# Performance work log

Measured on AMD Instinct MI355X. Metric: run time of the kernel, lower is better.

## Reference

```python
import jax, jax.numpy as jnp
import numpy as np


def setup_inputs() -> dict:
    key = jax.random.key(0)
    k1, k2, k3 = jax.random.split(key, 3)
    B, C, H, W = 64, 1024, 32, 32
    x = jax.random.normal(k1, (B, C, H, W), dtype=jnp.float32)
    # Conv2d(C, 1, kernel_size=1): weight [1, C, 1, 1] -> flatten to [C], bias [1] -> scalar
    bound = 1.0 / np.sqrt(C)
    attn_w = jax.random.uniform(k2, (C,), dtype=jnp.float32, minval=-bound, maxval=bound)
    attn_b = jax.random.uniform(k3, (), dtype=jnp.float32, minval=-bound, maxval=bound)
    return {"x": x, "attn_w": attn_w, "attn_b": attn_b}


def reference(x, attn_w, attn_b):
    B, C, H, W = x.shape
    # 1x1 conv producing one channel: score[b,h,w] = sum_c x[b,c,h,w]*w[c] + b
    scores = jnp.einsum('bchw,c->bhw', x, attn_w) + attn_b          # [B,H,W]
    attn = jax.nn.softmax(scores.reshape(B, -1), axis=-1)           # softmax over H*W
    attn = attn.reshape(B, H, W)
    # weighted sum pooling over spatial dims
    out = jnp.einsum('bchw,bhw->bc', x, attn)                       # [B,C]
    return out
```

## Files before the change

### kernel.cpp

```cpp
#include <hip/hip_runtime.h>

#define NB 64
#define NC 1024
#define NHW 1024
#define NCHUNK 16
#define CCH 64

__device__ inline float wave_reduce_max(float v) {
    #pragma unroll
    for (int off = 32; off; off >>= 1) v = fmaxf(v, __shfl_xor(v, off));
    return v;
}
__device__ inline float wave_reduce_sum(float v) {
    #pragma unroll
    for (int off = 32; off; off >>= 1) v += __shfl_xor(v, off);
    return v;
}

__global__ __launch_bounds__(256) void scores_partial_kernel(
        const float* __restrict__ x, const float* __restrict__ w,
        float* __restrict__ partials) {
    const int tid   = threadIdx.x;
    const int b     = blockIdx.x >> 4;
    const int chunk = blockIdx.x & 15;
    const int c0    = chunk * CCH;
    const float* xb = x + ((size_t)(b * NC + c0)) * NHW + tid * 4;

    float4 ps = {0.f, 0.f, 0.f, 0.f};
    #pragma unroll 8
    for (int k = 0; k < CCH; ++k) {
        const float4 v = *reinterpret_cast<const float4*>(xb + (size_t)k * NHW);
        const float wk = w[c0 + k];
        ps.x += v.x * wk; ps.y += v.y * wk;
        ps.z += v.z * wk; ps.w += v.w * wk;
    }
    reinterpret_cast<float4*>(partials + (size_t)blockIdx.x * NHW)[tid] = ps;
}

__global__ __launch_bounds__(256) void softmax_kernel(
        const float* __restrict__ partials, float* __restrict__ attn) {
    __shared__ float redm[4];
    __shared__ float reds[4];
    const int tid  = threadIdx.x;
    const int wave = tid >> 6, lane = tid & 63;
    const int b    = blockIdx.x;

    float4 s = {0.f, 0.f, 0.f, 0.f};
    #pragma unroll
    for (int i = 0; i < NCHUNK; ++i) {
        const float4 p = reinterpret_cast<const float4*>(
            partials + (size_t)(b * NCHUNK + i) * NHW)[tid];
        s.x += p.x; s.y += p.y; s.z += p.z; s.w += p.w;
    }

    float m = fmaxf(fmaxf(s.x, s.y), fmaxf(s.z, s.w));
    m = wave_reduce_max(m);
    if (lane == 0) redm[wave] = m;
    __syncthreads();
    m = fmaxf(fmaxf(redm[0], redm[1]), fmaxf(redm[2], redm[3]));

    float4 e;
    e.x = __expf(s.x - m); e.y = __expf(s.y - m);
    e.z = __expf(s.z - m); e.w = __expf(s.w - m);
    float z = e.x + e.y + e.z + e.w;
    z = wave_reduce_sum(z);
    if (lane == 0) reds[wave] = z;
    __syncthreads();
    const float inv = 1.0f / (reds[0] + reds[1] + reds[2] + reds[3]);

    e.x *= inv; e.y *= inv; e.z *= inv; e.w *= inv;
    reinterpret_cast<float4*>(attn + (size_t)b * NHW)[tid] = e;
}

__global__ __launch_bounds__(256) void pool_kernel(
        const float* __restrict__ x, const float* __restrict__ attn,
        float* __restrict__ out) {
    const int rbid = (NB * NC / 4 - 1) - blockIdx.x;
    const int wave = threadIdx.x >> 6;
    const int lane = threadIdx.x & 63;
    const int out_idx = (rbid << 2) + wave;
    const int b = out_idx >> 10;
    const float4* xr = reinterpret_cast<const float4*>(x + (size_t)out_idx * NHW);
    const float4* ar = reinterpret_cast<const float4*>(attn + (size_t)b * NHW);

    float acc = 0.0f;
    #pragma unroll
    for (int i = 0; i < 4; ++i) {
        const float4 xv = xr[(i << 6) + lane];
        const float4 av = ar[(i << 6) + lane];
        acc += xv.x * av.x + xv.y * av.y + xv.z * av.z + xv.w * av.w;
    }
    acc = wave_reduce_sum(acc);
    if (lane == 0) out[out_idx] = acc;
}

extern "C" void kernel_launch(void* const* d_in, const int* in_sizes, int n_in,
                              void* d_out, int out_size, void* d_ws, size_t ws_size,
                              hipStream_t stream) {
    const float* x = (const float*)d_in[0];
    const float* w = (const float*)d_in[1];
    float* out      = (float*)d_out;
    float* partials = (float*)d_ws;
    float* attn     = partials + (size_t)NB * NCHUNK * NHW;

    scores_partial_kernel<<<NB * NCHUNK, 256, 0, stream>>>(x, w, partials);
    softmax_kernel<<<NB, 256, 0, stream>>>(partials, attn);
    pool_kernel<<<(NB * NC) / 4, 256, 0, stream>>>(x, attn, out);
}
```

Baseline: 85.14 us.

## Software-pipeline scores, softmax and pooling across batch groups in fused launches

Result: slower. 113.3 us (+33.0%).

```diff
diff --git a/kernel.cpp b/kernel.cpp
--- a/kernel.cpp
+++ b/kernel.cpp
@@ -3,95 +3,96 @@
 #define NB 64
 #define NC 1024
 #define NHW 1024
-#define NCHUNK 16
-#define CCH 64
+#define GRP 16
+#define NSCH 64
+#define SCH (NC / NSCH)
+#define S_BLOCKS (GRP * NSCH)
+#define P_BLOCKS (GRP * (NC / 4))
+#define M_BLOCKS GRP
 
+__device__ inline float wave_reduce_sum(float v) {
+    #pragma unroll
+    for (int off = 32; off; off >>= 1) v += __shfl_xor(v, off);
+    return v;
+}
 __device__ inline float wave_reduce_max(float v) {
     #pragma unroll
     for (int off = 32; off; off >>= 1) v = fmaxf(v, __shfl_xor(v, off));
     return v;
 }
-__device__ inline float wave_reduce_sum(float v) {
-    #pragma unroll
-    for (int off = 32; off; off >>= 1) v += __shfl_xor(v, off);
-    return v;
-}
 
-__global__ __launch_bounds__(256) void scores_partial_kernel(
+__global__ __launch_bounds__(256) void stage_kernel(
         const float* __restrict__ x, const float* __restrict__ w,
-        float* __restrict__ partials) {
-    const int tid   = threadIdx.x;
-    const int b     = blockIdx.x >> 4;
-    const int chunk = blockIdx.x & 15;
-    const int c0    = chunk * CCH;
-    const float* xb = x + ((size_t)(b * NC + c0)) * NHW + tid * 4;
-
-    float4 ps = {0.f, 0.f, 0.f, 0.f};
-    #pragma unroll 8
-    for (int k = 0; k < CCH; ++k) {
-        const float4 v = *reinterpret_cast<const float4*>(xb + (size_t)k * NHW);
-        const float wk = w[c0 + k];
-        ps.x += v.x * wk; ps.y += v.y * wk;
-        ps.z += v.z * wk; ps.w += v.w * wk;
-    }
-    reinterpret_cast<float4*>(partials + (size_t)blockIdx.x * NHW)[tid] = ps;
-}
-
-__global__ __launch_bounds__(256) void softmax_kernel(
-        const float* __restrict__ partials, float* __restrict__ attn) {
-    __shared__ float redm[4];
-    __shared__ float reds[4];
+        float* __restrict__ partials, float* __restrict__ attn,
+        float* __restrict__ out, int sg, int pg, int mg, int nS, int nP) {
+    __shared__ float redm[4], reds[4];
     const int tid  = threadIdx.x;
     const int wave = tid >> 6, lane = tid & 63;
-    const int b    = blockIdx.x;
+    int bid = blockIdx.x;
 
-    float4 s = {0.f, 0.f, 0.f, 0.f};
-    #pragma unroll
-    for (int i = 0; i < NCHUNK; ++i) {
-        const float4 p = reinterpret_cast<const float4*>(
-            partials + (size_t)(b * NCHUNK + i) * NHW)[tid];
-        s.x += p.x; s.y += p.y; s.z += p.z; s.w += p.w;
+    if (bid < nS) {
+        const int b     = sg * GRP + (bid >> 6);
+        const int chunk = bid & 63;
+        const int c0    = chunk * SCH;
+        const float* xb = x + ((size_t)(b * NC + c0)) * NHW + tid * 4;
+        float4 ps = {0.f, 0.f, 0.f, 0.f};
+        #pragma unroll
+        for (int k = 0; k < SCH; ++k) {
+            const float4 v = *reinterpret_cast<const float4*>(xb + (size_t)k * NHW);
+            const float wk = w[c0 + k];
+            ps.x += v.x * wk; ps.y += v.y * wk;
+            ps.z += v.z * wk; ps.w += v.w * wk;
+        }
+        reinterpret_cast<float4*>(
+            partials + ((size_t)b * NSCH + chunk) * NHW)[tid] = ps;
+        return;
     }
-
-    float m = fmaxf(fmaxf(s.x, s.y), fmaxf(s.z, s.w));
-    m = wave_reduce_max(m);
-    if (lane == 0) redm[wave] = m;
-    __syncthreads();
-    m = fmaxf(fmaxf(redm[0], redm[1]), fmaxf(redm[2], redm[3]));
-
-    float4 e;
-    e.x = __expf(s.x - m); e.y = __expf(s.y - m);
-    e.z = __expf(s.z - m); e.w = __expf(s.w - m);
-    float z = e.x + e.y + e.z + e.w;
-    z = wave_reduce_sum(z);
-    if (lane == 0) reds[wave] = z;
-    __syncthreads();
-    const float inv = 1.0f / (reds[0] + reds[1] + reds[2] + reds[3]);
-
-    e.x *= inv; e.y *= inv; e.z *= inv; e.w *= inv;
-    reinterpret_cast<float4*>(attn + (size_t)b * NHW)[tid] = e;
-}
-
-__global__ __launch_bounds__(256) void pool_kernel(
-        const float* __restrict__ x, const float* __restrict__ attn,
-        float* __restrict__ out) {
-    const int rbid = (NB * NC / 4 - 1) - blockIdx.x;
-    const int wave = threadIdx.x >> 6;
-    const int lane = threadIdx.x & 63;
-    const int out_idx = (rbid << 2) + wave;
-    const int b = out_idx >> 10;
-    const float4* xr = reinterpret_cast<const float4*>(x + (size_t)out_idx * NHW);
-    const float4* ar = reinterpret_cast<const float4*>(attn + (size_t)b * NHW);
-
-    float acc = 0.0f;
-    #pragma unroll
-    for (int i = 0; i < 4; ++i) {
-        const float4 xv = xr[(i << 6) + lane];
-        const float4 av = ar[(i << 6) + lane];
-        acc += xv.x * av.x + xv.y * av.y + xv.z * av.z + xv.w * av.w;
+    bid -= nS;
+    if (bid < nP) {
+        const int b = pg * GRP + (bid >> 8);
+        const int c = (bid & 255) * 4 + wave;
+        const float4* xr = reinterpret_cast<const float4*>(
+            x + ((size_t)(b * NC + c)) * NHW);
+        const float4* ar = reinterpret_cast<const float4*>(
+            attn + (size_t)b * NHW);
+        float acc = 0.f;
+        #pragma unroll
+        for (int q = 0; q < 4; ++q) {
+            const float4 xv = xr[(q << 6) + lane];
+            const float4 av = ar[(q << 6) + lane];
+            acc += xv.x * av.x + xv.y * av.y + xv.z * av.z + xv.w * av.w;
+        }
+        acc = wave_reduce_sum(acc);
+        if (lane == 0) out[b * NC + c] = acc;
+        return;
     }
-    acc = wave_reduce_sum(acc);
-    if (lane == 0) out[out_idx] = acc;
+    bid -= nP;
+    {
+        const int b = mg * GRP + bid;
+        const float4* pb = reinterpret_cast<const float4*>(
+            partials + (size_t)b * NSCH * NHW);
+        float4 s = {0.f, 0.f, 0.f, 0.f};
+        #pragma unroll 8
+        for (int k = 0; k < NSCH; ++k) {
+            const float4 p = pb[k * (NHW / 4) + tid];
+            s.x += p.x; s.y += p.y; s.z += p.z; s.w += p.w;
+        }
+        float m = fmaxf(fmaxf(s.x, s.y), fmaxf(s.z, s.w));
+        m = wave_reduce_max(m);
+        if (lane == 0) redm[wave] = m;
+        __syncthreads();
+        m = fmaxf(fmaxf(redm[0], redm[1]), fmaxf(redm[2], redm[3]));
+        float4 e;
+        e.x = __expf(s.x - m); e.y = __expf(s.y - m);
+        e.z = __expf(s.z - m); e.w = __expf(s.w - m);
+        float z = e.x + e.y + e.z + e.w;
+        z = wave_reduce_sum(z);
+        if (lane == 0) reds[wave] = z;
+        __syncthreads();
+        const float inv = 1.0f / (reds[0] + reds[1] + reds[2] + reds[3]);
+        e.x *= inv; e.y *= inv; e.z *= inv; e.w *= inv;
+        reinterpret_cast<float4*>(attn + (size_t)b * NHW)[tid] = e;
+    }
 }
 
 extern "C" void kernel_launch(void* const* d_in, const int* in_sizes, int n_in,
@@ -101,9 +102,23 @@
     const float* w = (const float*)d_in[1];
     float* out      = (float*)d_out;
     float* partials = (float*)d_ws;
-    float* attn     = partials + (size_t)NB * NCHUNK * NHW;
+    float* attn     = partials + (size_t)NB * NSCH * NHW;
 
-    scores_partial_kernel<<<NB * NCHUNK, 256, 0, stream>>>(x, w, partials);
-    softmax_kernel<<<NB, 256, 0, stream>>>(partials, attn);
-    pool_kernel<<<(NB * NC) / 4, 256, 0, stream>>>(x, attn, out);
+    struct Step { int sg, pg, mg; };
+    const Step steps[6] = {
+        { 0, -1, -1},
+        { 1, -1,  0},
+        { 2,  0,  1},
+        { 3,  1,  2},
+        {-1,  2,  3},
+        {-1,  3, -1},
+    };
+    for (int i = 0; i < 6; ++i) {
+        const int nS = steps[i].sg >= 0 ? S_BLOCKS : 0;
+        const int nP = steps[i].pg >= 0 ? P_BLOCKS : 0;
+        const int nM = steps[i].mg >= 0 ? M_BLOCKS : 0;
+        stage_kernel<<<nS + nP + nM, 256, 0, stream>>>(
+            x, w, partials, attn, out,
+            steps[i].sg, steps[i].pg, steps[i].mg, nS, nP);
+    }
 }
```

## Write an fp16 copy of x during scoring and pool from it

Applied to the files above, without the earlier changes.

Result: slower. 100.2 us (+17.7%).

```diff
diff --git a/kernel.cpp b/kernel.cpp
--- a/kernel.cpp
+++ b/kernel.cpp
@@ -1,30 +1,33 @@
 #include <hip/hip_runtime.h>
+#include <hip/hip_fp16.h>
 
 #define NB 64
 #define NC 1024
 #define NHW 1024
 #define NCHUNK 16
-#define CCH 64
+#define CCH (NC / NCHUNK)
 
+__device__ inline float wave_reduce_sum(float v) {
+    #pragma unroll
+    for (int off = 32; off; off >>= 1) v += __shfl_xor(v, off);
+    return v;
+}
 __device__ inline float wave_reduce_max(float v) {
     #pragma unroll
     for (int off = 32; off; off >>= 1) v = fmaxf(v, __shfl_xor(v, off));
     return v;
 }
-__device__ inline float wave_reduce_sum(float v) {
-    #pragma unroll
-    for (int off = 32; off; off >>= 1) v += __shfl_xor(v, off);
-    return v;
-}
 
-__global__ __launch_bounds__(256) void scores_partial_kernel(
+__global__ __launch_bounds__(256) void score_copy_kernel(
         const float* __restrict__ x, const float* __restrict__ w,
-        float* __restrict__ partials) {
+        __half* __restrict__ xh, float* __restrict__ partials) {
     const int tid   = threadIdx.x;
     const int b     = blockIdx.x >> 4;
     const int chunk = blockIdx.x & 15;
     const int c0    = chunk * CCH;
-    const float* xb = x + ((size_t)(b * NC + c0)) * NHW + tid * 4;
+    const size_t base = ((size_t)(b * NC + c0)) * NHW + tid * 4;
+    const float* xb = x + base;
+    __half* hb      = xh + base;
 
     float4 ps = {0.f, 0.f, 0.f, 0.f};
     #pragma unroll 8
@@ -33,14 +36,17 @@
         const float wk = w[c0 + k];
         ps.x += v.x * wk; ps.y += v.y * wk;
         ps.z += v.z * wk; ps.w += v.w * wk;
+        __half2 h01 = __floats2half2_rn(v.x, v.y);
+        __half2 h23 = __floats2half2_rn(v.z, v.w);
+        *reinterpret_cast<__half2*>(hb + (size_t)k * NHW)     = h01;
+        *reinterpret_cast<__half2*>(hb + (size_t)k * NHW + 2) = h23;
     }
     reinterpret_cast<float4*>(partials + (size_t)blockIdx.x * NHW)[tid] = ps;
 }
 
 __global__ __launch_bounds__(256) void softmax_kernel(
         const float* __restrict__ partials, float* __restrict__ attn) {
-    __shared__ float redm[4];
-    __shared__ float reds[4];
+    __shared__ float redm[4], reds[4];
     const int tid  = threadIdx.x;
     const int wave = tid >> 6, lane = tid & 63;
     const int b    = blockIdx.x;
@@ -52,13 +58,11 @@
             partials + (size_t)(b * NCHUNK + i) * NHW)[tid];
         s.x += p.x; s.y += p.y; s.z += p.z; s.w += p.w;
     }
-
     float m = fmaxf(fmaxf(s.x, s.y), fmaxf(s.z, s.w));
     m = wave_reduce_max(m);
     if (lane == 0) redm[wave] = m;
     __syncthreads();
     m = fmaxf(fmaxf(redm[0], redm[1]), fmaxf(redm[2], redm[3]));
-
     float4 e;
     e.x = __expf(s.x - m); e.y = __expf(s.y - m);
     e.z = __expf(s.z - m); e.w = __expf(s.w - m);
@@ -67,28 +71,40 @@
     if (lane == 0) reds[wave] = z;
     __syncthreads();
     const float inv = 1.0f / (reds[0] + reds[1] + reds[2] + reds[3]);
-
     e.x *= inv; e.y *= inv; e.z *= inv; e.w *= inv;
     reinterpret_cast<float4*>(attn + (size_t)b * NHW)[tid] = e;
 }
 
-__global__ __launch_bounds__(256) void pool_kernel(
-        const float* __restrict__ x, const float* __restrict__ attn,
+__global__ __launch_bounds__(256) void pool_half_kernel(
+        const __half* __restrict__ xh, const float* __restrict__ attn,
         float* __restrict__ out) {
     const int rbid = (NB * NC / 4 - 1) - blockIdx.x;
     const int wave = threadIdx.x >> 6;
     const int lane = threadIdx.x & 63;
     const int out_idx = (rbid << 2) + wave;
     const int b = out_idx >> 10;
-    const float4* xr = reinterpret_cast<const float4*>(x + (size_t)out_idx * NHW);
+
+    const uint4* hr = reinterpret_cast<const uint4*>(xh + (size_t)out_idx * NHW);
     const float4* ar = reinterpret_cast<const float4*>(attn + (size_t)b * NHW);
+    const uint4 ha = hr[2 * lane];
+    const uint4 hbv = hr[2 * lane + 1];
+    float4 a0 = ar[4 * lane + 0], a1 = ar[4 * lane + 1];
+    float4 a2 = ar[4 * lane + 2], a3 = ar[4 * lane + 3];
 
-    float acc = 0.0f;
-    #pragma unroll
-    for (int i = 0; i < 4; ++i) {
-        const float4 xv = xr[(i << 6) + lane];
-        const float4 av = ar[(i << 6) + lane];
-        acc += xv.x * av.x + xv.y * av.y + xv.z * av.z + xv.w * av.w;
+    const __half2* h2a = reinterpret_cast<const __half2*>(&ha);
+    const __half2* h2b = reinterpret_cast<const __half2*>(&hbv);
+    float acc = 0.f;
+    {
+        float2 f0 = __half22float2(h2a[0]), f1 = __half22float2(h2a[1]);
+        float2 f2 = __half22float2(h2a[2]), f3 = __half22float2(h2a[3]);
+        acc += f0.x * a0.x + f0.y * a0.y + f1.x * a0.z + f1.y * a0.w;
+        acc += f2.x * a1.x + f2.y * a1.y + f3.x * a1.z + f3.y * a1.w;
+    }
+    {
+        float2 f0 = __half22float2(h2b[0]), f1 = __half22float2(h2b[1]);
+        float2 f2 = __half22float2(h2b[2]), f3 = __half22float2(h2b[3]);
+        acc += f0.x * a2.x + f0.y * a2.y + f1.x * a2.z + f1.y * a2.w;
+        acc += f2.x * a3.x + f2.y * a3.y + f3.x * a3.z + f3.y * a3.w;
     }
     acc = wave_reduce_sum(acc);
     if (lane == 0) out[out_idx] = acc;
@@ -100,10 +116,11 @@
     const float* x = (const float*)d_in[0];
     const float* w = (const float*)d_in[1];
     float* out      = (float*)d_out;
-    float* partials = (float*)d_ws;
+    __half* xh      = (__half*)d_ws;
+    float* partials = (float*)(xh + (size_t)NB * NC * NHW);
     float* attn     = partials + (size_t)NB * NCHUNK * NHW;
 
-    scores_partial_kernel<<<NB * NCHUNK, 256, 0, stream>>>(x, w, partials);
+    score_copy_kernel<<<NB * NCHUNK, 256, 0, stream>>>(x, w, xh, partials);
     softmax_kernel<<<NB, 256, 0, stream>>>(partials, attn);
-    pool_kernel<<<(NB * NC) / 4, 256, 0, stream>>>(x, attn, out);
+    pool_half_kernel<<<(NB * NC) / 4, 256, 0, stream>>>(xh, attn, out);
 }
```
